# Kernel optimization log

Hardware: AMD Instinct MI355X
Metric: run time of the kernel (lower is better)

The kernel has to match this reference:

```python
import jax, jax.numpy as jnp
import numpy as np

N = 4096          # num_nodes
E = 65536         # num edges (avg degree 16)
WALK_LENGTH = 16
OUT_DIM = 8


def setup_inputs() -> dict:
    key = jax.random.key(0)
    k1, k2 = jax.random.split(key, 2)
    edge_index = jax.random.randint(k1, (2, E), 0, N, dtype=jnp.int64)
    # nn.Linear(walk_length, out_dim): weight [out_dim, walk_length], bias [out_dim]
    linear_w = (jax.random.normal(k2, (OUT_DIM, WALK_LENGTH), jnp.float32)
                / np.float32(np.sqrt(WALK_LENGTH)))
    linear_b = jnp.zeros((OUT_DIM,), jnp.float32)
    return {"edge_index": edge_index, "num_nodes": N,
            "linear_w": linear_w, "linear_b": linear_b}


def reference(edge_index, num_nodes, linear_w, linear_b):
    row, col = edge_index[0], edge_index[1]
    # out-degree via scatter_add, clamped to >= 1
    deg = jnp.zeros((num_nodes,), jnp.float32).at[row].add(1.0)
    deg = jnp.maximum(deg, 1.0)
    rw_values = 1.0 / deg[row]                              # [E]
    # random-walk transition matrix P[row, col] = 1/deg[row]
    # (.at[].add sums duplicate edges, matching coalesce())
    P = jnp.zeros((num_nodes, num_nodes), jnp.float32).at[row, col].add(rw_values)
    Pt = P.T

    def step(cur, _):
        cur = Pt @ cur                                      # [N, N]
        return cur, jnp.diagonal(cur)                       # k-step return probs

    cur0 = jnp.eye(num_nodes, dtype=jnp.float32)
    _, diags = jax.lax.scan(step, cur0, None, length=WALK_LENGTH)
    rw_diag = diags.T                                       # [N, walk_length]
    return rw_diag @ linear_w.T + linear_b                  # [N, out_dim]
```

## Files before the change

kernel.cpp:

```cpp
#include <hip/hip_runtime.h>
#include <hip/hip_fp16.h>
#include <hip/hip_fp8.h>

#define NNODES 4096
#define LWALK 16
#define ODIM 8

#define FP8_SCALE 256.0f
#define FP8_INV   0.00390625f
#define FP8_INV2  1.52587890625e-05f

typedef unsigned int uint4n __attribute__((ext_vector_type(4)));
typedef unsigned int uint2n __attribute__((ext_vector_type(2)));
typedef float float2n __attribute__((ext_vector_type(2)));

__device__ __forceinline__ void dec8f(unsigned int lo, unsigned int hi, float* f) {
#if __has_builtin(__builtin_amdgcn_cvt_pk_f32_fp8)
    float2n p;
    p = __builtin_amdgcn_cvt_pk_f32_fp8((int)lo, false); f[0] = p.x; f[1] = p.y;
    p = __builtin_amdgcn_cvt_pk_f32_fp8((int)lo, true);  f[2] = p.x; f[3] = p.y;
    p = __builtin_amdgcn_cvt_pk_f32_fp8((int)hi, false); f[4] = p.x; f[5] = p.y;
    p = __builtin_amdgcn_cvt_pk_f32_fp8((int)hi, true);  f[6] = p.x; f[7] = p.y;
#else
    unsigned int w[2] = {lo, hi};
    const unsigned char* b = (const unsigned char*)w;
#pragma unroll
    for (int i = 0; i < 8; ++i) {
        __hip_fp8_e4m3 t; t.__x = b[i]; f[i] = (float)t;
    }
#endif
}

__device__ __forceinline__ void enc8f(const float* a, unsigned int* lo,
                                      unsigned int* hi) {
#if __has_builtin(__builtin_amdgcn_cvt_pk_fp8_f32)
    int l = 0, h = 0;
    l = __builtin_amdgcn_cvt_pk_fp8_f32(a[0], a[1], l, false);
    l = __builtin_amdgcn_cvt_pk_fp8_f32(a[2], a[3], l, true);
    h = __builtin_amdgcn_cvt_pk_fp8_f32(a[4], a[5], h, false);
    h = __builtin_amdgcn_cvt_pk_fp8_f32(a[6], a[7], h, true);
    *lo = (unsigned int)l; *hi = (unsigned int)h;
#else
    unsigned char b[8];
#pragma unroll
    for (int i = 0; i < 8; ++i)
        b[i] = __hip_cvt_float_to_fp8(a[i], __HIP_SATFINITE, __HIP_E4M3);
    unsigned int w[2];
    __builtin_memcpy(w, b, 8);
    *lo = w[0]; *hi = w[1];
#endif
}

__device__ __forceinline__ void dec16f(uint4n w, float* f) {
    dec8f(w.x, w.y, f);
    dec8f(w.z, w.w, f + 8);
}

__device__ __forceinline__ uint4n enc16f(const float* a) {
    uint4n o;
    unsigned int lo, hi;
    enc8f(a, &lo, &hi);     o.x = lo; o.y = hi;
    enc8f(a + 8, &lo, &hi); o.z = lo; o.w = hi;
    return o;
}

__global__ void detect_fmt_k(const void* ei, int E, int* flag) {
    if (blockIdx.x == 0 && threadIdx.x == 0) {
        const long long* p = (const long long*)ei;
        int ok = 1;
        for (int i = 0; i < 64; ++i) {
            long long v = p[i];
            if (v < 0 || v >= NNODES) { ok = 0; break; }
        }
        *flag = ok;
    }
}

__device__ __forceinline__ int load_idx(const void* p, int i, int fmt) {
    if (fmt) return (int)((const long long*)p)[i];
    return ((const int*)p)[i];
}

__global__ void build_deg_cnt_k(const void* ei, int E, int* deg, int* cnt,
                                const int* fmt) {
    int e = blockIdx.x * blockDim.x + threadIdx.x;
    if (e >= E) return;
    int f = *fmt;
    int r = load_idx(ei, e, f);
    int c = load_idx(ei, E + e, f);
    atomicAdd(&deg[r], 1);
    atomicAdd(&cnt[c], 1);
}

__global__ void scan_k(const int* __restrict__ cnt, int* __restrict__ rowptr,
                       int* __restrict__ cursor) {
    __shared__ int sm[1024];
    int tid = threadIdx.x;
    int v0 = (cnt[4 * tid + 0] + 3) & ~3;
    int v1 = (cnt[4 * tid + 1] + 3) & ~3;
    int v2 = (cnt[4 * tid + 2] + 3) & ~3;
    int v3 = (cnt[4 * tid + 3] + 3) & ~3;
    int tsum = v0 + v1 + v2 + v3;
    sm[tid] = tsum;
    __syncthreads();
    int val = tsum;
    for (int off = 1; off < 1024; off <<= 1) {
        int t = (tid >= off) ? sm[tid - off] : 0;
        __syncthreads();
        val += t;
        sm[tid] = val;
        __syncthreads();
    }
    int excl = val - tsum;
    int p0 = excl, p1 = excl + v0, p2 = p1 + v1, p3 = p2 + v2;
    rowptr[4 * tid + 0] = p0; rowptr[4 * tid + 1] = p1;
    rowptr[4 * tid + 2] = p2; rowptr[4 * tid + 3] = p3;
    cursor[4 * tid + 0] = p0; cursor[4 * tid + 1] = p1;
    cursor[4 * tid + 2] = p2; cursor[4 * tid + 3] = p3;
    if (tid == 1023) rowptr[4096] = val;
}

__global__ void fill_pad_k(const void* ei, int E, const int* __restrict__ deg,
                           int* cursor, const int* __restrict__ rowptr,
                           uint2* __restrict__ epad, const int* fmt) {
    int e = blockIdx.x * blockDim.x + threadIdx.x;
    if (e < E) {
        int f = *fmt;
        int r = load_idx(ei, e, f);
        int c = load_idx(ei, E + e, f);
        int pos = atomicAdd(&cursor[c], 1);
        int d = deg[r];
        float v = 1.0f / (float)(d < 1 ? 1 : d);
        epad[pos] = make_uint2((unsigned)r, __float_as_uint(v));
    }
}

__global__ void pad_fill_k(const int* __restrict__ rowptr,
                           const int* __restrict__ cursor,
                           uint2* __restrict__ epad) {
    int c = blockIdx.x * blockDim.x + threadIdx.x;
    if (c >= NNODES) return;
    for (int p = cursor[c]; p < rowptr[c + 1]; ++p)
        epad[p] = make_uint2(0u, 0u);
}

__global__ __launch_bounds__(256) void x2build_k(
    const int* __restrict__ rowptr, const uint2* __restrict__ epad,
    unsigned char* __restrict__ Y8, float* __restrict__ rw) {
    __shared__ float row[NNODES];
    __shared__ float dia1;
    const int c = blockIdx.x;
    const int t = threadIdx.x;
    for (int i = t; i < NNODES; i += 256) row[i] = 0.f;
    if (t == 0) dia1 = 0.f;
    __syncthreads();
    const int beg = rowptr[c], end = rowptr[c + 1];
    const int g = t >> 4;
    const int l = t & 15;
    for (int i1 = beg + g; i1 < end; i1 += 16) {
        uint2 e1 = epad[i1];
        float v = __uint_as_float(e1.y);
        if (v != 0.f) {
            int r = (int)e1.x;
            if (r == c && l == 0) atomicAdd(&dia1, v);
            int b2 = rowptr[r], n2 = rowptr[r + 1];
            for (int j = b2 + l; j < n2; j += 16) {
                uint2 e2 = epad[j];
                float w = __uint_as_float(e2.y);
                if (w != 0.f) atomicAdd(&row[e2.x], v * w);
            }
        }
    }
    __syncthreads();
    if (t == 0) {
        rw[c * LWALK + 0] = dia1;
        rw[c * LWALK + 1] = row[c];
    }
    float f[16];
    const int base = t * 16;
#pragma unroll
    for (int u = 0; u < 16; ++u) f[u] = row[base + u] * FP8_SCALE;
    uint4n o = enc16f(f);
    __builtin_nontemporal_store(o, (uint4n*)(Y8 + (size_t)c * NNODES + base));
}

__global__ __launch_bounds__(256) void fused8_k(
    const unsigned char* __restrict__ X8, unsigned char* __restrict__ Y8,
    const int* __restrict__ rowptr, const uint2* __restrict__ epad,
    float* __restrict__ rw, int kcol,
    const unsigned char* __restrict__ PA, const unsigned char* __restrict__ PB,
    int colO, int colE, int nspmm) {
    __shared__ __half bt[64][66];
    __shared__ __half ct[64][66];
    const int bid = blockIdx.x;
    if (bid < nspmm) {
        const int slab = (bid >> 1) & 3;
        const int cg = ((bid >> 3) << 1) | (bid & 1);
        const int lane = threadIdx.x & 63;
        const int c =
            __builtin_amdgcn_readfirstlane(cg * 4 + (threadIdx.x >> 6));
        const int colo = slab * 1024 + lane * 16;
        const unsigned char* Xs = X8 + colo;
        const int beg = rowptr[c], end = rowptr[c + 1];
        float a[16];
#pragma unroll
        for (int u = 0; u < 16; ++u) a[u] = 0.f;
        for (int e = beg; e < end; e += 4) {
            uint2 ed[4];
#pragma unroll
            for (int j = 0; j < 4; ++j) ed[j] = epad[e + j];
            uint4n x[4];
#pragma unroll
            for (int j = 0; j < 4; ++j)
                x[j] = *(const uint4n*)(Xs + (size_t)ed[j].x * NNODES);
#pragma unroll
            for (int j = 0; j < 4; ++j) {
                float v = __uint_as_float(ed[j].y);
                float f[16];
                dec16f(x[j], f);
#pragma unroll
                for (int u = 0; u < 16; ++u) a[u] = fmaf(f[u], v, a[u]);
            }
        }
        if ((c >> 10) == slab && lane == ((c & 1023) >> 4)) {
            float d = 0.f;
#pragma unroll
            for (int u = 0; u < 16; ++u)
                if ((c & 15) == u) d = a[u];
            rw[c * LWALK + kcol] = d * FP8_INV;
        }
        uint4n o = enc16f(a);
        __builtin_nontemporal_store(o, (uint4n*)(Y8 + (size_t)c * NNODES + colo));
    } else {
        const int pb = bid - nspmm;
        const int i0 = (pb & 63) * 64;
        const int Jbeg = (pb >> 6) * (NNODES / 16);
        const int Jend = Jbeg + (NNODES / 16);
        const int t = threadIdx.x;
        const int li = t >> 2;
        const int q = t & 3;
        const int c0 = q * 16;
        float accO = 0.f, accE = 0.f;
        for (int J = Jbeg; J < Jend; J += 64) {
            uint4n b16 = __builtin_nontemporal_load(
                (const uint4n*)(PB + (size_t)(J + li) * NNODES + i0 + c0));
            uint4n g16 = __builtin_nontemporal_load(
                (const uint4n*)(PA + (size_t)(J + li) * NNODES + i0 + c0));
            __syncthreads();
            float bf[16], gf[16];
            dec16f(b16, bf);
            dec16f(g16, gf);
#pragma unroll
            for (int s = 0; s < 16; ++s) {
                bt[c0 + s][li] = __float2half(bf[s]);
                ct[c0 + s][li] = __float2half(gf[s]);
            }
            __syncthreads();
            uint4n a16 = __builtin_nontemporal_load(
                (const uint4n*)(PA + (size_t)(i0 + li) * NNODES + J + c0));
            float af[16];
            dec16f(a16, af);
#pragma unroll
            for (int s = 0; s < 16; ++s) {
                accO = fmaf(af[s], __half2float(bt[li][c0 + s]), accO);
                accE = fmaf(af[s], __half2float(ct[li][c0 + s]), accE);
            }
        }
        accO += __shfl_xor(accO, 1);
        accO += __shfl_xor(accO, 2);
        accE += __shfl_xor(accE, 1);
        accE += __shfl_xor(accE, 2);
        if (q == 0) {
            atomicAdd(&rw[(i0 + li) * LWALK + colO], accO * FP8_INV2);
            atomicAdd(&rw[(i0 + li) * LWALK + colE], accE * FP8_INV2);
        }
    }
}

__global__ __launch_bounds__(256) void finale_k(
    const unsigned char* __restrict__ PA, const unsigned char* __restrict__ PB,
    float* __restrict__ rw, const float* __restrict__ W,
    const float* __restrict__ b, float* __restrict__ out, int npair) {
    __shared__ __half bt[64][66];
    __shared__ __half ct[64][66];
    const int bid = blockIdx.x;
    if (bid < npair) {
        const int pb = bid;
        const int i0 = (pb & 63) * 64;
        const int Jbeg = (pb >> 6) * (NNODES / 16);
        const int Jend = Jbeg + (NNODES / 16);
        const int t = threadIdx.x;
        const int li = t >> 2;
        const int q = t & 3;
        const int c0 = q * 16;
        float accO = 0.f, accE = 0.f;
        for (int J = Jbeg; J < Jend; J += 64) {
            uint4n b16 = __builtin_nontemporal_load(
                (const uint4n*)(PB + (size_t)(J + li) * NNODES + i0 + c0));
            uint4n g16 = __builtin_nontemporal_load(
                (const uint4n*)(PA + (size_t)(J + li) * NNODES + i0 + c0));
            __syncthreads();
            float bf[16], gf[16];
            dec16f(b16, bf);
            dec16f(g16, gf);
#pragma unroll
            for (int s = 0; s < 16; ++s) {
                bt[c0 + s][li] = __float2half(bf[s]);
                ct[c0 + s][li] = __float2half(gf[s]);
            }
            __syncthreads();
            uint4n a16 = __builtin_nontemporal_load(
                (const uint4n*)(PA + (size_t)(i0 + li) * NNODES + J + c0));
            float af[16];
            dec16f(a16, af);
#pragma unroll
            for (int s = 0; s < 16; ++s) {
                accO = fmaf(af[s], __half2float(bt[li][c0 + s]), accO);
                accE = fmaf(af[s], __half2float(ct[li][c0 + s]), accE);
            }
        }
        accO += __shfl_xor(accO, 1);
        accO += __shfl_xor(accO, 2);
        accE += __shfl_xor(accE, 1);
        accE += __shfl_xor(accE, 2);
        if (q == 0) {
            atomicAdd(&rw[(i0 + li) * LWALK + 14], accO * FP8_INV2);
            atomicAdd(&rw[(i0 + li) * LWALK + 15], accE * FP8_INV2);
        }
    }
}

__global__ void linear_k(const float* __restrict__ rw, const float* __restrict__ W,
                         const float* __restrict__ b, float* __restrict__ out) {
    int i = blockIdx.x * blockDim.x + threadIdx.x;
    if (i >= NNODES * ODIM) return;
    int s = i >> 3, d = i & 7;
    float acc = b[d];
#pragma unroll
    for (int k = 0; k < LWALK; ++k)
        acc = fmaf(rw[s * LWALK + k], W[d * LWALK + k], acc);
    out[i] = acc;
}

extern "C" void kernel_launch(void* const* d_in, const int* in_sizes, int n_in,
                              void* d_out, int out_size, void* d_ws, size_t ws_size,
                              hipStream_t stream) {
    const void* ei = d_in[0];
    int E = in_sizes[0] / 2;
    const float* W = (const float*)d_in[2];
    const float* bias = (const float*)d_in[3];
    float* out = (float*)d_out;

    char* ws = (char*)d_ws;
    size_t off = 0;
    auto alloc = [&](size_t bytes) -> char* {
        char* p = ws + off;
        off = (off + bytes + 255) & ~(size_t)255;
        return p;
    };
    int* flag = (int*)alloc(4);
    int* deg = (int*)alloc(NNODES * 4);
    int* cnt = (int*)alloc(NNODES * 4);
    int* rowptr = (int*)alloc((NNODES + 1) * 4);
    int* cursor = (int*)alloc(NNODES * 4);
    uint2* epad = (uint2*)alloc(((size_t)E + 4 * NNODES) * 8);
    float* rw = (float*)alloc(NNODES * LWALK * 4);
    unsigned char* A = (unsigned char*)alloc((size_t)NNODES * NNODES);
    unsigned char* B = (unsigned char*)alloc((size_t)NNODES * NNODES);
    unsigned char* C = (unsigned char*)alloc((size_t)NNODES * NNODES);

    (void)hipMemsetAsync(deg, 0, NNODES * 4, stream);
    (void)hipMemsetAsync(cnt, 0, NNODES * 4, stream);
    (void)hipMemsetAsync(rw, 0, NNODES * LWALK * 4, stream);
    detect_fmt_k<<<1, 64, 0, stream>>>(ei, E, flag);
    build_deg_cnt_k<<<(E + 255) / 256, 256, 0, stream>>>(ei, E, deg, cnt, flag);
    scan_k<<<1, 1024, 0, stream>>>(cnt, rowptr, cursor);
    fill_pad_k<<<(E + 255) / 256, 256, 0, stream>>>(ei, E, deg, cursor, rowptr,
                                                    epad, flag);
    pad_fill_k<<<(NNODES + 255) / 256, 256, 0, stream>>>(rowptr, cursor, epad);

    x2build_k<<<NNODES, 256, 0, stream>>>(rowptr, epad, A, rw);

    const int SG = 4096;
    fused8_k<<<SG, 256, 0, stream>>>(A, B, rowptr, epad, rw, 2, nullptr, nullptr, 0, 0, SG);
    fused8_k<<<SG, 256, 0, stream>>>(B, C, rowptr, epad, rw, 3, nullptr, nullptr, 0, 0, SG);
    fused8_k<<<SG, 256, 0, stream>>>(C, A, rowptr, epad, rw, 4, nullptr, nullptr, 0, 0, SG);
    fused8_k<<<SG + 1024, 256, 0, stream>>>(A, B, rowptr, epad, rw, 5, A, C, 8, 9, SG);
    fused8_k<<<SG + 1024, 256, 0, stream>>>(B, C, rowptr, epad, rw, 6, B, A, 10, 11, SG);
    fused8_k<<<SG + 1024, 256, 0, stream>>>(C, A, rowptr, epad, rw, 7, C, B, 12, 13, SG);
    finale_k<<<1024, 256, 0, stream>>>(A, C, rw, W, bias, out, 1024);
    linear_k<<<(NNODES * ODIM + 255) / 256, 256, 0, stream>>>(rw, W, bias, out);
}
```

Measured before the change: 297.8 us.

## Run the walk chain per 16-column slab in LDS and batch pair products

Replaces the per-step global fp8 SpMM launches with one persistent kernel in which each block owns a 16-column slab. The slab's powers up to step 8 stay double-buffered in 64KB of LDS, and the M4/M5/M7/M8 slabs are written out for the later diagonal-of-product terms. The two-hop start is built from an out-edge CSR. Edge weights are packed as fp16 alongside 16-bit indices, and the four pairwise diagonal products run in a single launch. This is meant to remove the dense global-memory traffic between steps and the per-step launches. In exchange it runs only 256 large-LDS blocks at one block per CU and adds an extra scan and CSR build.

```diff
diff --git a/kernel.cpp b/kernel.cpp
--- a/kernel.cpp
+++ b/kernel.cpp
@@ -11,7 +11,6 @@
 #define FP8_INV2  1.52587890625e-05f
 
 typedef unsigned int uint4n __attribute__((ext_vector_type(4)));
-typedef unsigned int uint2n __attribute__((ext_vector_type(2)));
 typedef float float2n __attribute__((ext_vector_type(2)));
 
 __device__ __forceinline__ void dec8f(unsigned int lo, unsigned int hi, float* f) {
@@ -62,6 +61,18 @@
     enc8f(a, &lo, &hi);     o.x = lo; o.y = hi;
     enc8f(a + 8, &lo, &hi); o.z = lo; o.w = hi;
     return o;
+}
+
+__device__ __forceinline__ unsigned char enc1f(float f) {
+#if __has_builtin(__builtin_amdgcn_cvt_pk_fp8_f32)
+    return (unsigned char)(__builtin_amdgcn_cvt_pk_fp8_f32(f, 0.f, 0, false) & 0xFF);
+#else
+    return __hip_cvt_float_to_fp8(f, __HIP_SATFINITE, __HIP_E4M3);
+#endif
+}
+
+__device__ __forceinline__ float decw(unsigned int packed) {
+    return __half2float(__ushort_as_half((unsigned short)(packed >> 16)));
 }
 
 __global__ void detect_fmt_k(const void* ei, int E, int* flag) {
@@ -121,212 +132,196 @@
 }
 
 __global__ void fill_pad_k(const void* ei, int E, const int* __restrict__ deg,
-                           int* cursor, const int* __restrict__ rowptr,
-                           uint2* __restrict__ epad, const int* fmt) {
+                           int* cursor, int* ocursor,
+                           unsigned int* __restrict__ ep4,
+                           unsigned int* __restrict__ oidx, const int* fmt) {
     int e = blockIdx.x * blockDim.x + threadIdx.x;
     if (e < E) {
         int f = *fmt;
         int r = load_idx(ei, e, f);
         int c = load_idx(ei, E + e, f);
-        int pos = atomicAdd(&cursor[c], 1);
         int d = deg[r];
         float v = 1.0f / (float)(d < 1 ? 1 : d);
-        epad[pos] = make_uint2((unsigned)r, __float_as_uint(v));
+        int pos = atomicAdd(&cursor[c], 1);
+        unsigned hv = (unsigned)__half_as_ushort(__float2half(v));
+        ep4[pos] = (hv << 16) | (unsigned)r;
+        int opos = atomicAdd(&ocursor[r], 1);
+        oidx[opos] = (unsigned)c;
     }
 }
 
 __global__ void pad_fill_k(const int* __restrict__ rowptr,
                            const int* __restrict__ cursor,
-                           uint2* __restrict__ epad) {
+                           unsigned int* __restrict__ ep4) {
     int c = blockIdx.x * blockDim.x + threadIdx.x;
     if (c >= NNODES) return;
     for (int p = cursor[c]; p < rowptr[c + 1]; ++p)
-        epad[p] = make_uint2(0u, 0u);
-}
-
-__global__ __launch_bounds__(256) void x2build_k(
-    const int* __restrict__ rowptr, const uint2* __restrict__ epad,
-    unsigned char* __restrict__ Y8, float* __restrict__ rw) {
-    __shared__ float row[NNODES];
-    __shared__ float dia1;
-    const int c = blockIdx.x;
+        ep4[p] = 0u;
+}
+
+__global__ __launch_bounds__(512, 1) void chain_k(
+    const int* __restrict__ rowptr, const unsigned int* __restrict__ ep4,
+    const int* __restrict__ orowptr, const int* __restrict__ ocursor,
+    const unsigned int* __restrict__ oidx, const int* __restrict__ deg,
+    float* __restrict__ rw,
+    unsigned char* __restrict__ M4, unsigned char* __restrict__ M5,
+    unsigned char* __restrict__ M7, unsigned char* __restrict__ M8) {
+    __shared__ unsigned char bufA[NNODES * 16];
+    __shared__ unsigned char bufB[NNODES * 16];
     const int t = threadIdx.x;
-    for (int i = t; i < NNODES; i += 256) row[i] = 0.f;
-    if (t == 0) dia1 = 0.f;
-    __syncthreads();
-    const int beg = rowptr[c], end = rowptr[c + 1];
+    const int bid = blockIdx.x;
+    const int slab = (bid & 7) * 32 + (bid >> 3);
+    const int S0 = slab * 16;
+
+    float* col32 = (float*)bufB;
     const int g = t >> 4;
     const int l = t & 15;
-    for (int i1 = beg + g; i1 < end; i1 += 16) {
-        uint2 e1 = epad[i1];
-        float v = __uint_as_float(e1.y);
-        if (v != 0.f) {
-            int r = (int)e1.x;
-            if (r == c && l == 0) atomicAdd(&dia1, v);
-            int b2 = rowptr[r], n2 = rowptr[r + 1];
-            for (int j = b2 + l; j < n2; j += 16) {
-                uint2 e2 = epad[j];
-                float w = __uint_as_float(e2.y);
-                if (w != 0.f) atomicAdd(&row[e2.x], v * w);
+    for (int cl = 0; cl < 16; ++cl) {
+        const int gc = S0 + cl;
+        for (int i = t; i < NNODES; i += 512) col32[i] = 0.f;
+        __syncthreads();
+        const int dg = deg[gc];
+        const float vg = 1.f / (float)(dg < 1 ? 1 : dg);
+        const int ob = orowptr[gc], oe = ocursor[gc];
+        for (int p1 = ob + g; p1 < oe; p1 += 32) {
+            int m = (int)oidx[p1];
+            if (m == gc && l == 0)
+                atomicAdd(&rw[gc * LWALK + 0], vg);
+            int dm = deg[m];
+            float vm = vg / (float)(dm < 1 ? 1 : dm);
+            int mb = orowptr[m], me = ocursor[m];
+            for (int p2 = mb + l; p2 < me; p2 += 16)
+                atomicAdd(&col32[oidx[p2]], vm);
+        }
+        __syncthreads();
+        if (t == 0) rw[gc * LWALK + 1] = col32[gc];
+        for (int i = t; i < NNODES; i += 512)
+            bufA[i * 16 + cl] = enc1f(col32[i] * FP8_SCALE);
+        __syncthreads();
+    }
+
+    int rpb[8], rpe[8];
+#pragma unroll
+    for (int j = 0; j < 8; ++j) {
+        rpb[j] = rowptr[t + 512 * j];
+        rpe[j] = rowptr[t + 512 * j + 1];
+    }
+#pragma unroll 1
+    for (int k = 3; k <= 8; ++k) {
+        const unsigned char* src = (k & 1) ? bufA : bufB;
+        unsigned char* dst = (k & 1) ? bufB : bufA;
+        __syncthreads();
+#pragma unroll 1
+        for (int j = 0; j < 8; ++j) {
+            const int c = t + 512 * j;
+            float acc[16];
+#pragma unroll
+            for (int u = 0; u < 16; ++u) acc[u] = 0.f;
+            for (int e = rpb[j]; e < rpe[j]; e += 4) {
+                uint4n ew = *(const uint4n*)(ep4 + e);
+                uint4n x0 = *(const uint4n*)(src + (ew.x & 0xFFFFu) * 16);
+                uint4n x1 = *(const uint4n*)(src + (ew.y & 0xFFFFu) * 16);
+                uint4n x2 = *(const uint4n*)(src + (ew.z & 0xFFFFu) * 16);
+                uint4n x3 = *(const uint4n*)(src + (ew.w & 0xFFFFu) * 16);
+                float f[16];
+                float v;
+                v = decw(ew.x);
+                dec16f(x0, f);
+#pragma unroll
+                for (int u = 0; u < 16; ++u) acc[u] = fmaf(f[u], v, acc[u]);
+                v = decw(ew.y);
+                dec16f(x1, f);
+#pragma unroll
+                for (int u = 0; u < 16; ++u) acc[u] = fmaf(f[u], v, acc[u]);
+                v = decw(ew.z);
+                dec16f(x2, f);
+#pragma unroll
+                for (int u = 0; u < 16; ++u) acc[u] = fmaf(f[u], v, acc[u]);
+                v = decw(ew.w);
+                dec16f(x3, f);
+#pragma unroll
+                for (int u = 0; u < 16; ++u) acc[u] = fmaf(f[u], v, acc[u]);
             }
-        }
-    }
-    __syncthreads();
-    if (t == 0) {
-        rw[c * LWALK + 0] = dia1;
-        rw[c * LWALK + 1] = row[c];
-    }
-    float f[16];
-    const int base = t * 16;
-#pragma unroll
-    for (int u = 0; u < 16; ++u) f[u] = row[base + u] * FP8_SCALE;
-    uint4n o = enc16f(f);
-    __builtin_nontemporal_store(o, (uint4n*)(Y8 + (size_t)c * NNODES + base));
-}
-
-__global__ __launch_bounds__(256) void fused8_k(
-    const unsigned char* __restrict__ X8, unsigned char* __restrict__ Y8,
-    const int* __restrict__ rowptr, const uint2* __restrict__ epad,
-    float* __restrict__ rw, int kcol,
-    const unsigned char* __restrict__ PA, const unsigned char* __restrict__ PB,
-    int colO, int colE, int nspmm) {
+            if ((unsigned)(c - S0) < 16u) {
+                float d = 0.f;
+#pragma unroll
+                for (int u = 0; u < 16; ++u)
+                    if (c - S0 == u) d = acc[u];
+                rw[c * LWALK + (k - 1)] = d * FP8_INV;
+            }
+            uint4n o = enc16f(acc);
+            *(uint4n*)(dst + c * 16) = o;
+        }
+        __syncthreads();
+        if (k == 4 || k == 5 || k == 7 || k == 8) {
+            unsigned char* M = (k == 4) ? M4 : (k == 5) ? M5 : (k == 7) ? M7 : M8;
+#pragma unroll 1
+            for (int j = 0; j < 8; ++j) {
+                const int c = t + 512 * j;
+                uint4n o = *(const uint4n*)(dst + c * 16);
+                *(uint4n*)(M + (size_t)c * NNODES + S0) = o;
+            }
+        }
+    }
+}
+
+__global__ __launch_bounds__(256) void pairall_k(
+    const unsigned char* __restrict__ M4, const unsigned char* __restrict__ M5,
+    const unsigned char* __restrict__ M7, const unsigned char* __restrict__ M8,
+    float* __restrict__ rw) {
     __shared__ __half bt[64][66];
     __shared__ __half ct[64][66];
     const int bid = blockIdx.x;
-    if (bid < nspmm) {
-        const int slab = (bid >> 1) & 3;
-        const int cg = ((bid >> 3) << 1) | (bid & 1);
-        const int lane = threadIdx.x & 63;
-        const int c =
-            __builtin_amdgcn_readfirstlane(cg * 4 + (threadIdx.x >> 6));
-        const int colo = slab * 1024 + lane * 16;
-        const unsigned char* Xs = X8 + colo;
-        const int beg = rowptr[c], end = rowptr[c + 1];
-        float a[16];
-#pragma unroll
-        for (int u = 0; u < 16; ++u) a[u] = 0.f;
-        for (int e = beg; e < end; e += 4) {
-            uint2 ed[4];
-#pragma unroll
-            for (int j = 0; j < 4; ++j) ed[j] = epad[e + j];
-            uint4n x[4];
-#pragma unroll
-            for (int j = 0; j < 4; ++j)
-                x[j] = *(const uint4n*)(Xs + (size_t)ed[j].x * NNODES);
-#pragma unroll
-            for (int j = 0; j < 4; ++j) {
-                float v = __uint_as_float(ed[j].y);
-                float f[16];
-                dec16f(x[j], f);
-#pragma unroll
-                for (int u = 0; u < 16; ++u) a[u] = fmaf(f[u], v, a[u]);
-            }
-        }
-        if ((c >> 10) == slab && lane == ((c & 1023) >> 4)) {
-            float d = 0.f;
-#pragma unroll
-            for (int u = 0; u < 16; ++u)
-                if ((c & 15) == u) d = a[u];
-            rw[c * LWALK + kcol] = d * FP8_INV;
-        }
-        uint4n o = enc16f(a);
-        __builtin_nontemporal_store(o, (uint4n*)(Y8 + (size_t)c * NNODES + colo));
-    } else {
-        const int pb = bid - nspmm;
-        const int i0 = (pb & 63) * 64;
-        const int Jbeg = (pb >> 6) * (NNODES / 16);
-        const int Jend = Jbeg + (NNODES / 16);
-        const int t = threadIdx.x;
-        const int li = t >> 2;
-        const int q = t & 3;
-        const int c0 = q * 16;
-        float accO = 0.f, accE = 0.f;
-        for (int J = Jbeg; J < Jend; J += 64) {
-            uint4n b16 = __builtin_nontemporal_load(
-                (const uint4n*)(PB + (size_t)(J + li) * NNODES + i0 + c0));
-            uint4n g16 = __builtin_nontemporal_load(
-                (const uint4n*)(PA + (size_t)(J + li) * NNODES + i0 + c0));
-            __syncthreads();
-            float bf[16], gf[16];
-            dec16f(b16, bf);
-            dec16f(g16, gf);
-#pragma unroll
-            for (int s = 0; s < 16; ++s) {
-                bt[c0 + s][li] = __float2half(bf[s]);
-                ct[c0 + s][li] = __float2half(gf[s]);
-            }
-            __syncthreads();
-            uint4n a16 = __builtin_nontemporal_load(
-                (const uint4n*)(PA + (size_t)(i0 + li) * NNODES + J + c0));
-            float af[16];
-            dec16f(a16, af);
-#pragma unroll
-            for (int s = 0; s < 16; ++s) {
-                accO = fmaf(af[s], __half2float(bt[li][c0 + s]), accO);
-                accE = fmaf(af[s], __half2float(ct[li][c0 + s]), accE);
-            }
-        }
-        accO += __shfl_xor(accO, 1);
-        accO += __shfl_xor(accO, 2);
-        accE += __shfl_xor(accE, 1);
-        accE += __shfl_xor(accE, 2);
-        if (q == 0) {
-            atomicAdd(&rw[(i0 + li) * LWALK + colO], accO * FP8_INV2);
-            atomicAdd(&rw[(i0 + li) * LWALK + colE], accE * FP8_INV2);
-        }
-    }
-}
-
-__global__ __launch_bounds__(256) void finale_k(
-    const unsigned char* __restrict__ PA, const unsigned char* __restrict__ PB,
-    float* __restrict__ rw, const float* __restrict__ W,
-    const float* __restrict__ b, float* __restrict__ out, int npair) {
-    __shared__ __half bt[64][66];
-    __shared__ __half ct[64][66];
-    const int bid = blockIdx.x;
-    if (bid < npair) {
-        const int pb = bid;
-        const int i0 = (pb & 63) * 64;
-        const int Jbeg = (pb >> 6) * (NNODES / 16);
-        const int Jend = Jbeg + (NNODES / 16);
-        const int t = threadIdx.x;
-        const int li = t >> 2;
-        const int q = t & 3;
-        const int c0 = q * 16;
-        float accO = 0.f, accE = 0.f;
-        for (int J = Jbeg; J < Jend; J += 64) {
-            uint4n b16 = __builtin_nontemporal_load(
-                (const uint4n*)(PB + (size_t)(J + li) * NNODES + i0 + c0));
-            uint4n g16 = __builtin_nontemporal_load(
-                (const uint4n*)(PA + (size_t)(J + li) * NNODES + i0 + c0));
-            __syncthreads();
-            float bf[16], gf[16];
-            dec16f(b16, bf);
-            dec16f(g16, gf);
-#pragma unroll
-            for (int s = 0; s < 16; ++s) {
-                bt[c0 + s][li] = __float2half(bf[s]);
-                ct[c0 + s][li] = __float2half(gf[s]);
-            }
-            __syncthreads();
-            uint4n a16 = __builtin_nontemporal_load(
-                (const uint4n*)(PA + (size_t)(i0 + li) * NNODES + J + c0));
-            float af[16];
-            dec16f(a16, af);
-#pragma unroll
-            for (int s = 0; s < 16; ++s) {
-                accO = fmaf(af[s], __half2float(bt[li][c0 + s]), accO);
-                accE = fmaf(af[s], __half2float(ct[li][c0 + s]), accE);
-            }
-        }
-        accO += __shfl_xor(accO, 1);
-        accO += __shfl_xor(accO, 2);
-        accE += __shfl_xor(accE, 1);
-        accE += __shfl_xor(accE, 2);
-        if (q == 0) {
-            atomicAdd(&rw[(i0 + li) * LWALK + 14], accO * FP8_INV2);
-            atomicAdd(&rw[(i0 + li) * LWALK + 15], accE * FP8_INV2);
-        }
+    const int grp = bid >> 10;
+    const int pb = bid & 1023;
+    const unsigned char* PA;
+    const unsigned char* PB1;
+    const unsigned char* PB2;
+    int colO, colE;
+    if (grp == 0)      { PA = M5; PB1 = M4; PB2 = M5; colO = 8;  colE = 9;  }
+    else if (grp == 1) { PA = M7; PB1 = M4; PB2 = M7; colO = 10; colE = 13; }
+    else if (grp == 2) { PA = M8; PB1 = M4; PB2 = M8; colO = 11; colE = 15; }
+    else               { PA = M8; PB1 = M5; PB2 = M7; colO = 12; colE = 14; }
+    const int i0 = (pb & 63) * 64;
+    const int Jbeg = (pb >> 6) * (NNODES / 16);
+    const int Jend = Jbeg + (NNODES / 16);
+    const int t = threadIdx.x;
+    const int li = t >> 2;
+    const int q = t & 3;
+    const int c0 = q * 16;
+    float accO = 0.f, accE = 0.f;
+    for (int J = Jbeg; J < Jend; J += 64) {
+        uint4n b16 = __builtin_nontemporal_load(
+            (const uint4n*)(PB1 + (size_t)(J + li) * NNODES + i0 + c0));
+        uint4n g16 = __builtin_nontemporal_load(
+            (const uint4n*)(PB2 + (size_t)(J + li) * NNODES + i0 + c0));
+        __syncthreads();
+        float bf[16], gf[16];
+        dec16f(b16, bf);
+        dec16f(g16, gf);
+#pragma unroll
+        for (int s = 0; s < 16; ++s) {
+            bt[c0 + s][li] = __float2half(bf[s]);
+            ct[c0 + s][li] = __float2half(gf[s]);
+        }
+        __syncthreads();
+        uint4n a16 = __builtin_nontemporal_load(
+            (const uint4n*)(PA + (size_t)(i0 + li) * NNODES + J + c0));
+        float af[16];
+        dec16f(a16, af);
+#pragma unroll
+        for (int s = 0; s < 16; ++s) {
+            accO = fmaf(af[s], __half2float(bt[li][c0 + s]), accO);
+            accE = fmaf(af[s], __half2float(ct[li][c0 + s]), accE);
+        }
+    }
+    accO += __shfl_xor(accO, 1);
+    accO += __shfl_xor(accO, 2);
+    accE += __shfl_xor(accE, 1);
+    accE += __shfl_xor(accE, 2);
+    if (q == 0) {
+        atomicAdd(&rw[(i0 + li) * LWALK + colO], accO * FP8_INV2);
+        atomicAdd(&rw[(i0 + li) * LWALK + colE], accE * FP8_INV2);
     }
 }
 
@@ -363,11 +358,15 @@
     int* cnt = (int*)alloc(NNODES * 4);
     int* rowptr = (int*)alloc((NNODES + 1) * 4);
     int* cursor = (int*)alloc(NNODES * 4);
-    uint2* epad = (uint2*)alloc(((size_t)E + 4 * NNODES) * 8);
+    int* orowptr = (int*)alloc((NNODES + 1) * 4);
+    int* ocursor = (int*)alloc(NNODES * 4);
+    unsigned int* ep4 = (unsigned int*)alloc(((size_t)E + 4 * NNODES) * 4);
+    unsigned int* oidx = (unsigned int*)alloc(((size_t)E + 4 * NNODES) * 4);
     float* rw = (float*)alloc(NNODES * LWALK * 4);
-    unsigned char* A = (unsigned char*)alloc((size_t)NNODES * NNODES);
-    unsigned char* B = (unsigned char*)alloc((size_t)NNODES * NNODES);
-    unsigned char* C = (unsigned char*)alloc((size_t)NNODES * NNODES);
+    unsigned char* M4 = (unsigned char*)alloc((size_t)NNODES * NNODES);
+    unsigned char* M5 = (unsigned char*)alloc((size_t)NNODES * NNODES);
+    unsigned char* M7 = (unsigned char*)alloc((size_t)NNODES * NNODES);
+    unsigned char* M8 = (unsigned char*)alloc((size_t)NNODES * NNODES);
 
     (void)hipMemsetAsync(deg, 0, NNODES * 4, stream);
     (void)hipMemsetAsync(cnt, 0, NNODES * 4, stream);
@@ -375,19 +374,15 @@
     detect_fmt_k<<<1, 64, 0, stream>>>(ei, E, flag);
     build_deg_cnt_k<<<(E + 255) / 256, 256, 0, stream>>>(ei, E, deg, cnt, flag);
     scan_k<<<1, 1024, 0, stream>>>(cnt, rowptr, cursor);
-    fill_pad_k<<<(E + 255) / 256, 256, 0, stream>>>(ei, E, deg, cursor, rowptr,
-                                                    epad, flag);
-    pad_fill_k<<<(NNODES + 255) / 256, 256, 0, stream>>>(rowptr, cursor, epad);
-
-    x2build_k<<<NNODES, 256, 0, stream>>>(rowptr, epad, A, rw);
-
-    const int SG = 4096;
-    fused8_k<<<SG, 256, 0, stream>>>(A, B, rowptr, epad, rw, 2, nullptr, nullptr, 0, 0, SG);
-    fused8_k<<<SG, 256, 0, stream>>>(B, C, rowptr, epad, rw, 3, nullptr, nullptr, 0, 0, SG);
-    fused8_k<<<SG, 256, 0, stream>>>(C, A, rowptr, epad, rw, 4, nullptr, nullptr, 0, 0, SG);
-    fused8_k<<<SG + 1024, 256, 0, stream>>>(A, B, rowptr, epad, rw, 5, A, C, 8, 9, SG);
-    fused8_k<<<SG + 1024, 256, 0, stream>>>(B, C, rowptr, epad, rw, 6, B, A, 10, 11, SG);
-    fused8_k<<<SG + 1024, 256, 0, stream>>>(C, A, rowptr, epad, rw, 7, C, B, 12, 13, SG);
-    finale_k<<<1024, 256, 0, stream>>>(A, C, rw, W, bias, out, 1024);
+    scan_k<<<1, 1024, 0, stream>>>(deg, orowptr, ocursor);
+    fill_pad_k<<<(E + 255) / 256, 256, 0, stream>>>(ei, E, deg, cursor, ocursor,
+                                                    ep4, oidx, flag);
+    pad_fill_k<<<(NNODES + 255) / 256, 256, 0, stream>>>(rowptr, cursor, ep4);
+
+    chain_k<<<256, 512, 0, stream>>>(rowptr, ep4, orowptr, ocursor, oidx, deg,
+                                     rw, M4, M5, M7, M8);
+
+    pairall_k<<<4096, 256, 0, stream>>>(M4, M5, M7, M8, rw);
+
     linear_k<<<(NNODES * ODIM + 255) / 256, 256, 0, stream>>>(rw, W, bias, out);
 }
```

New measurement: 357.9 us. +20.2%, slower.
